# Kernel tuning notes

Measured on AMD Instinct MI355X. Metric: run time of the kernel, lower is better.

Reference implementation:

```python
import jax, jax.numpy as jnp
import numpy as np
import math

B, D_MODEL, H, D_K, L = 24, 128, 8, 16, 512


def setup_inputs() -> dict:
    key = jax.random.key(0)
    ks = jax.random.split(key, 5)
    x = jax.random.normal(ks[0], (B, D_MODEL, L), dtype=jnp.float32)
    Wq = jax.random.normal(ks[1], (H, B, D_K, D_MODEL), dtype=jnp.float32)
    Wk = jax.random.normal(ks[2], (H, B, D_K, D_MODEL), dtype=jnp.float32)
    Wv = jax.random.normal(ks[3], (H, B, D_K, D_MODEL), dtype=jnp.float32)
    Wo = jax.random.normal(ks[4], (B, H * D_K, D_MODEL), dtype=jnp.float32)
    return {"x": x, "Wq": Wq, "Wk": Wk, "Wv": Wv, "Wo": Wo}


def reference(x, Wq, Wk, Wv, Wo):
    # Per-head, per-batch projections: [h,b,k,d] @ [b,d,l] -> [h,b,k,l]
    Q = jnp.einsum('hbkd,bdl->hbkl', Wq, x)
    K = jnp.einsum('hbkd,bdl->hbkl', Wk, x)
    V = jnp.einsum('hbkd,bdl->hbkl', Wv, x)
    # scores[h,b,l,m] = Q[:, :, :, l] . K[:, :, :, m]; torch softmax dim=1 of
    # the [B, L, L] score -> softmax over the QUERY axis l (axis=2 here).
    scores = jnp.einsum('hbkl,hbkm->hblm', Q, K) / math.sqrt(D_K)
    attn = jax.nn.softmax(scores, axis=2)
    # head_i = V @ attn : [h,b,v,l] @ [h,b,l,m] -> [h,b,v,m]
    heads = jnp.einsum('hbvl,hblm->hbvm', V, attn)
    # concat heads along channel dim: [b, h*v, L]
    head = heads.transpose(1, 0, 2, 3).reshape(B, H * D_K, L)
    # out = Wo @ head : [b, h*v, d_model] treated as [b,128,128] @ [b,128,L]
    out = jnp.einsum('bod,bdl->bol', Wo, head)
    return out
```

## Files before the change

### kernel.cpp

```cpp
#include <hip/hip_runtime.h>
#include <math.h>

#define NB 24
#define DM 128
#define NH 8
#define DK 16
#define LL 512
#define HB (NH * NB)

#define XTH_OFF 0
#define XTL_OFF 3145728
#define WHI_OFF 6291456
#define WLO_OFF 8650752
#define WOB_OFF 11010048
#define QB_OFF  11796480
#define KB_OFF  18087936
#define VB_OFF  24379392
#define HT_OFF  27525120

typedef __attribute__((ext_vector_type(8))) short bf16x8;
typedef __attribute__((ext_vector_type(4))) float f32x4;
typedef __attribute__((ext_vector_type(4))) int   i32x4;

#define MFMA  __builtin_amdgcn_mfma_f32_16x16x32_bf16
#define EXP2  __builtin_amdgcn_exp2f
#define BPERM __builtin_amdgcn_ds_bpermute

static __device__ __forceinline__ unsigned bfr(float x) {
    return (__float_as_uint(x) + 0x8000u) & 0xffff0000u;
}
static __device__ __forceinline__ unsigned pk2(unsigned e, unsigned o) {
    return (e >> 16) | o;
}

__global__ __launch_bounds__(256)
void prep(const float* __restrict__ x,
          const float* __restrict__ Wq,
          const float* __restrict__ Wk,
          const float* __restrict__ Wv,
          const float* __restrict__ Wo,
          unsigned short* __restrict__ xthi,
          unsigned short* __restrict__ xtlo,
          unsigned short* __restrict__ whi,
          unsigned short* __restrict__ wlo,
          unsigned short* __restrict__ wob)
{
    __shared__ float T[128][65];
    const int bid = blockIdx.x, tid = threadIdx.x;

    if (bid < 192) {
        const int b = bid >> 3, lc = bid & 7;
        const float* __restrict__ xb = x + (size_t)b * 65536 + lc * 64;
        #pragma unroll
        for (int i = 0; i < 32; ++i) {
            const int idx = i * 256 + tid;
            T[idx >> 6][idx & 63] = xb[(size_t)(idx >> 6) * LL + (idx & 63)];
        }
        __syncthreads();
        #pragma unroll
        for (int i = 0; i < 32; ++i) {
            const int idx = i * 256 + tid;
            const int l = idx >> 7, d = idx & 127;
            const float v = T[d][l];
            const unsigned h = bfr(v);
            const size_t o = (size_t)b * 65536 + (size_t)(lc * 64 + l) * DM + d;
            xthi[o] = (unsigned short)(h >> 16);
            xtlo[o] = (unsigned short)(bfr(v - __uint_as_float(h)) >> 16);
        }
    } else if (bid < 768) {
        const int w = bid - 192, hb = w / 3, mat = w - hb * 3;
        const float* __restrict__ src =
            (mat == 0 ? Wq : (mat == 1 ? Wk : Wv)) + (size_t)hb * 2048;
        unsigned short* __restrict__ dh = whi + (size_t)w * 2048;
        unsigned short* __restrict__ dl = wlo + (size_t)w * 2048;
        for (int i = tid; i < 2048; i += 256) {
            const float v = src[i];
            const unsigned h = bfr(v);
            dh[i] = (unsigned short)(h >> 16);
            dl[i] = (unsigned short)(bfr(v - __uint_as_float(h)) >> 16);
        }
    } else {
        const int w = bid - 768;
        const float* __restrict__ src = Wo + (size_t)w * 4096;
        unsigned short* __restrict__ d = wob + (size_t)w * 4096;
        for (int i = tid; i < 4096; i += 256)
            d[i] = (unsigned short)(bfr(src[i]) >> 16);
    }
}

__global__ __launch_bounds__(256)
void qkv_mfma(const unsigned short* __restrict__ xthi,
              const unsigned short* __restrict__ xtlo,
              const unsigned short* __restrict__ whi,
              const unsigned short* __restrict__ wlo,
              unsigned short* __restrict__ qb,
              unsigned short* __restrict__ kb,
              unsigned short* __restrict__ vb)
{
    const int blk  = blockIdx.x;
    const int nc   = blk & 1;
    const int hm   = blk >> 1;
    const int mat  = hm % 3;
    const int hb   = hm / 3;
    const int b    = hb % NB;
    const int wv   = threadIdx.x >> 6;
    const int lane = threadIdx.x & 63;
    const int g = lane >> 4, mR = lane & 15;
    const int l0 = nc * 256 + wv * 64;

    const unsigned short* __restrict__ wA = whi + (size_t)hm * 2048 + mR * 128 + g * 8;
    const unsigned short* __restrict__ wB = wlo + (size_t)hm * 2048 + mR * 128 + g * 8;
    const unsigned short* __restrict__ xh = xthi + (size_t)b * 65536 + g * 8;
    const unsigned short* __restrict__ xl = xtlo + (size_t)b * 65536 + g * 8;

    f32x4 C[4];
    #pragma unroll
    for (int t = 0; t < 4; ++t) C[t] = (f32x4){0.f, 0.f, 0.f, 0.f};

    #pragma unroll
    for (int kk = 0; kk < 4; ++kk) {
        const bf16x8 aH = *(const bf16x8*)(wA + kk * 32);
        const bf16x8 aL = *(const bf16x8*)(wB + kk * 32);
        #pragma unroll
        for (int t = 0; t < 4; ++t) {
            const size_t lo_ = (size_t)(l0 + t * 16 + mR) * DM + kk * 32;
            const bf16x8 bH = *(const bf16x8*)(xh + lo_);
            const bf16x8 bL = *(const bf16x8*)(xl + lo_);
            C[t] = MFMA(aH, bH, C[t], 0, 0, 0);
            C[t] = MFMA(aH, bL, C[t], 0, 0, 0);
            C[t] = MFMA(aL, bH, C[t], 0, 0, 0);
        }
    }

    if (mat == 2) {
        unsigned short* __restrict__ vo = vb + (size_t)hb * 8192;
        #pragma unroll
        for (int t = 0; t < 4; ++t) {
            const int l = l0 + t * 16 + mR;
            #pragma unroll
            for (int i = 0; i < 4; ++i)
                vo[(size_t)(4 * g + i) * LL + l] =
                    (unsigned short)(bfr(C[t][i]) >> 16);
        }
    } else {
        const float scale = (mat == 1) ? (0.25f * 1.44269504f) : 1.0f;
        unsigned short* __restrict__ dst =
            (mat == 0 ? qb : kb) + (size_t)hb * LL * 32;
        #pragma unroll
        for (int t = 0; t < 4; ++t) {
            const int l = l0 + t * 16 + mR;
            ushort4 hi4, lo4;
            #pragma unroll
            for (int i = 0; i < 4; ++i) {
                const float v = C[t][i] * scale;
                const unsigned h = bfr(v);
                const unsigned lw = bfr(v - __uint_as_float(h));
                ((unsigned short*)&hi4)[i] = (unsigned short)(h >> 16);
                ((unsigned short*)&lo4)[i] = (unsigned short)(lw >> 16);
            }
            *(ushort4*)(dst + (size_t)l * 32 + 4 * g)      = hi4;
            *(ushort4*)(dst + (size_t)l * 32 + 16 + 4 * g) = lo4;
        }
    }
}

static __device__ __forceinline__ void soft_pv(
    const f32x4& s0, const f32x4& s1, float tm, float& bar, float& sm,
    f32x4& O, const bf16x8& aV, int aLo, int aHi, bool up)
{
    const float nb = fmaxf(bar, tm + 32.f);
    const float f  = EXP2(bar - nb);
    bar = nb;
    const unsigned u0 = bfr(EXP2(s0[0]-nb)), u1 = bfr(EXP2(s0[1]-nb));
    const unsigned u2 = bfr(EXP2(s0[2]-nb)), u3 = bfr(EXP2(s0[3]-nb));
    const unsigned w0 = bfr(EXP2(s1[0]-nb)), w1 = bfr(EXP2(s1[1]-nb));
    const unsigned w2 = bfr(EXP2(s1[2]-nb)), w3 = bfr(EXP2(s1[3]-nb));
    const float sacc =
        ((__uint_as_float(u0) + __uint_as_float(u1)) +
         (__uint_as_float(u2) + __uint_as_float(u3))) +
        ((__uint_as_float(w0) + __uint_as_float(w1)) +
         (__uint_as_float(w2) + __uint_as_float(w3)));
    sm = fmaf(sm, f, sacc);
    O *= f;
    const int c0 = (int)pk2(u0, u1), c1 = (int)pk2(u2, u3);
    const int c2 = (int)pk2(w0, w1), c3 = (int)pk2(w2, w3);
    const int p00 = BPERM(aLo, c0), p02 = BPERM(aLo, c2);
    const int p10 = BPERM(aLo, c1), p12 = BPERM(aLo, c3);
    const int p20 = BPERM(aHi, c0), p22 = BPERM(aHi, c2);
    const int p30 = BPERM(aHi, c1), p32 = BPERM(aHi, c3);
    i32x4 bi = { up ? p00 : p02, up ? p10 : p12,
                 up ? p20 : p22, up ? p30 : p32 };
    O = MFMA(aV, __builtin_bit_cast(bf16x8, bi), O, 0, 0, 0);
}

__global__ __launch_bounds__(256)
void attn_mfma(const unsigned short* __restrict__ qb,
               const unsigned short* __restrict__ kb,
               const unsigned short* __restrict__ vb,
               unsigned short* __restrict__ ht)
{
    const int hb   = blockIdx.x >> 2;
    const int mc   = blockIdx.x & 3;
    const int tid  = threadIdx.x;
    const int wave = tid >> 6;
    const int lane = tid & 63;
    const int g    = lane >> 4;
    const int mR   = lane & 15;
    const int mb   = mc * 128 + wave * 32;

    const unsigned short* Kr0 = kb + ((size_t)hb * LL + mb + mR) * 32;
    const unsigned short* Kr1 = Kr0 + 16 * 32;
    const bf16x8 bK0  = *(const bf16x8*)(Kr0 + g * 8);
    const bf16x8 bK0s = *(const bf16x8*)(Kr0 + (g ^ 2) * 8);
    const bf16x8 bK1  = *(const bf16x8*)(Kr1 + g * 8);
    const bf16x8 bK1s = *(const bf16x8*)(Kr1 + (g ^ 2) * 8);

    const unsigned short* qrow = qb + ((size_t)hb * LL + mR) * 32 + g * 8;
    const unsigned short* vrow = vb + ((size_t)hb * DK + mR) * LL + g * 8;

    f32x4 O0 = {0.f,0.f,0.f,0.f}, O1 = {0.f,0.f,0.f,0.f};
    float bar0 = -1e30f, bar1 = -1e30f, sm0 = 0.f, sm1 = 0.f;

    const int aLo = ((g & 1) * 32 + mR) * 4;
    const int aHi = aLo + 64;
    const bool up = (g < 2);

    for (int l = 0; l < LL; l += 32) {
        const bf16x8 aQ0 = *(const bf16x8*)(qrow + (size_t)l * 32);
        const bf16x8 aQ1 = *(const bf16x8*)(qrow + (size_t)(l + 16) * 32);

        const f32x4 z = {0.f,0.f,0.f,0.f};
        f32x4 sA0 = MFMA(aQ0, bK0, z, 0,0,0);  sA0 = MFMA(aQ0, bK0s, sA0, 0,0,0);
        f32x4 sB0 = MFMA(aQ0, bK1, z, 0,0,0);  sB0 = MFMA(aQ0, bK1s, sB0, 0,0,0);
        f32x4 sA1 = MFMA(aQ1, bK0, z, 0,0,0);  sA1 = MFMA(aQ1, bK0s, sA1, 0,0,0);
        f32x4 sB1 = MFMA(aQ1, bK1, z, 0,0,0);  sB1 = MFMA(aQ1, bK1s, sB1, 0,0,0);

        float tmA = fmaxf(fmaxf(fmaxf(sA0[0],sA0[1]), fmaxf(sA0[2],sA0[3])),
                          fmaxf(fmaxf(sA1[0],sA1[1]), fmaxf(sA1[2],sA1[3])));
        float tmB = fmaxf(fmaxf(fmaxf(sB0[0],sB0[1]), fmaxf(sB0[2],sB0[3])),
                          fmaxf(fmaxf(sB1[0],sB1[1]), fmaxf(sB1[2],sB1[3])));
        tmA = fmaxf(tmA, __shfl_xor(tmA, 16, 64));
        tmA = fmaxf(tmA, __shfl_xor(tmA, 32, 64));
        tmB = fmaxf(tmB, __shfl_xor(tmB, 16, 64));
        tmB = fmaxf(tmB, __shfl_xor(tmB, 32, 64));

        if (__any(tmA + 64.f > bar0) || __any(tmB + 64.f > bar1)) {
            const bf16x8 aV = *(const bf16x8*)(vrow + l);
            soft_pv(sA0, sA1, tmA, bar0, sm0, O0, aV, aLo, aHi, up);
            soft_pv(sB0, sB1, tmB, bar1, sm1, O1, aV, aLo, aHi, up);
        }
    }

    sm0 += __shfl_xor(sm0, 16, 64);  sm0 += __shfl_xor(sm0, 32, 64);
    sm1 += __shfl_xor(sm1, 16, 64);  sm1 += __shfl_xor(sm1, 32, 64);
    const float i0 = 1.f / sm0, i1 = 1.f / sm1;

    const int h = hb / NB, bb = hb % NB;
    unsigned short* __restrict__ ho =
        ht + (size_t)bb * 65536 + (size_t)(mb + mR) * DM + h * 16 + 4 * g;
    ushort4 p0, p1;
    #pragma unroll
    for (int i = 0; i < 4; ++i) {
        ((unsigned short*)&p0)[i] = (unsigned short)(bfr(O0[i] * i0) >> 16);
        ((unsigned short*)&p1)[i] = (unsigned short)(bfr(O1[i] * i1) >> 16);
    }
    *(ushort4*)ho              = p0;
    *(ushort4*)(ho + 16 * DM)  = p1;
}

__global__ __launch_bounds__(256)
void out_mfma(const unsigned short* __restrict__ wob,
              const unsigned short* __restrict__ ht,
              float* __restrict__ out)
{
    const int blk  = blockIdx.x;
    const int b    = blk >> 5;
    const int mq   = (blk >> 4) & 1;
    const int nq   = blk & 15;
    const int wv   = threadIdx.x >> 6;
    const int lane = threadIdx.x & 63;
    const int g = lane >> 4, mR = lane & 15;
    const int m0 = (mq * 4 + wv) * 16;
    const int n0 = nq * 32;

    const unsigned short* __restrict__ A =
        wob + (size_t)b * 16384 + (size_t)(m0 + mR) * DM + g * 8;
    const unsigned short* __restrict__ B = ht + (size_t)b * 65536 + g * 8;

    f32x4 C0 = {0.f,0.f,0.f,0.f}, C1 = {0.f,0.f,0.f,0.f};
    #pragma unroll
    for (int kk = 0; kk < 4; ++kk) {
        const bf16x8 aW = *(const bf16x8*)(A + kk * 32);
        const bf16x8 b0 = *(const bf16x8*)(B + (size_t)(n0 + mR) * DM + kk * 32);
        const bf16x8 b1 = *(const bf16x8*)(B + (size_t)(n0 + 16 + mR) * DM + kk * 32);
        C0 = MFMA(aW, b0, C0, 0, 0, 0);
        C1 = MFMA(aW, b1, C1, 0, 0, 0);
    }

    float* __restrict__ ob = out + (size_t)b * 65536 + (size_t)(m0 + 4 * g) * LL;
    #pragma unroll
    for (int i = 0; i < 4; ++i) {
        ob[(size_t)i * LL + n0 + mR]      = C0[i];
        ob[(size_t)i * LL + n0 + 16 + mR] = C1[i];
    }
}

extern "C" void kernel_launch(void* const* d_in, const int* in_sizes, int n_in,
                              void* d_out, int out_size, void* d_ws, size_t ws_size,
                              hipStream_t stream) {
    const float* x  = (const float*)d_in[0];
    const float* Wq = (const float*)d_in[1];
    const float* Wk = (const float*)d_in[2];
    const float* Wv = (const float*)d_in[3];
    const float* Wo = (const float*)d_in[4];
    float* out = (float*)d_out;

    char* ws = (char*)d_ws;
    unsigned short* xthi = (unsigned short*)(ws + XTH_OFF);
    unsigned short* xtlo = (unsigned short*)(ws + XTL_OFF);
    unsigned short* whi  = (unsigned short*)(ws + WHI_OFF);
    unsigned short* wlo  = (unsigned short*)(ws + WLO_OFF);
    unsigned short* wob  = (unsigned short*)(ws + WOB_OFF);
    unsigned short* qb   = (unsigned short*)(ws + QB_OFF);
    unsigned short* kb   = (unsigned short*)(ws + KB_OFF);
    unsigned short* vb   = (unsigned short*)(ws + VB_OFF);
    unsigned short* ht   = (unsigned short*)(ws + HT_OFF);

    prep     <<<864,     256, 0, stream>>>(x, Wq, Wk, Wv, Wo, xthi, xtlo, whi, wlo, wob);
    qkv_mfma <<<HB * 6,  256, 0, stream>>>(xthi, xtlo, whi, wlo, qb, kb, vb);
    attn_mfma<<<HB * 4,  256, 0, stream>>>(qb, kb, vb, ht);
    out_mfma <<<NB * 32, 256, 0, stream>>>(wob, ht, out);
}
```

Measured before the change: 127.3 us.

## Fuse weight bf16 splitting into GEMMs and use two-pass exact softmax max

Stops pre-converting Wq/Wk/Wv/Wo in the prep kernel. The QKV and output GEMM kernels now load the fp32 weights directly and split or convert them to bf16 in registers, which removes the weight workspace traffic and shrinks prep to the x transpose only. The x transpose now uses a smaller LDS tile and packed 32-bit stores. Attention replaces the online-rescaled softmax with its conditional skip by a first pass that computes the exact column max from cheap scores, then a second pass doing exp, a packed v_cvt_pk_bf16_f32 conversion and the PV MFMA without bpermute shuffles. The price is recomputing QK scores twice and redundant weight conversion across blocks.

```diff
diff --git a/kernel.cpp b/kernel.cpp
--- a/kernel.cpp
+++ b/kernel.cpp
@@ -10,13 +10,10 @@
 
 #define XTH_OFF 0
 #define XTL_OFF 3145728
-#define WHI_OFF 6291456
-#define WLO_OFF 8650752
-#define WOB_OFF 11010048
-#define QB_OFF  11796480
-#define KB_OFF  18087936
-#define VB_OFF  24379392
-#define HT_OFF  27525120
+#define QB_OFF  6291456
+#define KB_OFF  12582912
+#define VB_OFF  18874368
+#define HT_OFF  22020096
 
 typedef __attribute__((ext_vector_type(8))) short bf16x8;
 typedef __attribute__((ext_vector_type(4))) float f32x4;
@@ -24,75 +21,78 @@
 
 #define MFMA  __builtin_amdgcn_mfma_f32_16x16x32_bf16
 #define EXP2  __builtin_amdgcn_exp2f
-#define BPERM __builtin_amdgcn_ds_bpermute
 
 static __device__ __forceinline__ unsigned bfr(float x) {
     return (__float_as_uint(x) + 0x8000u) & 0xffff0000u;
 }
-static __device__ __forceinline__ unsigned pk2(unsigned e, unsigned o) {
-    return (e >> 16) | o;
+
+static __device__ __forceinline__ unsigned cvtpk(float a, float b) {
+    unsigned r;
+    asm("v_cvt_pk_bf16_f32 %0, %1, %2" : "=v"(r) : "v"(a), "v"(b));
+    return r;
+}
+
+static __device__ __forceinline__ void wsplit(const float* __restrict__ p,
+                                              bf16x8& aH, bf16x8& aL) {
+    const float4 f0 = *(const float4*)p;
+    const float4 f1 = *(const float4*)(p + 4);
+    const float f[8] = {f0.x, f0.y, f0.z, f0.w, f1.x, f1.y, f1.z, f1.w};
+    i32x4 h, l;
+    #pragma unroll
+    for (int q = 0; q < 4; ++q) {
+        const unsigned h0 = bfr(f[2 * q]), h1 = bfr(f[2 * q + 1]);
+        const unsigned e0 = bfr(f[2 * q]     - __uint_as_float(h0));
+        const unsigned e1 = bfr(f[2 * q + 1] - __uint_as_float(h1));
+        h[q] = (int)((h0 >> 16) | (h1 & 0xffff0000u));
+        l[q] = (int)((e0 >> 16) | (e1 & 0xffff0000u));
+    }
+    aH = __builtin_bit_cast(bf16x8, h);
+    aL = __builtin_bit_cast(bf16x8, l);
 }
 
 __global__ __launch_bounds__(256)
 void prep(const float* __restrict__ x,
-          const float* __restrict__ Wq,
-          const float* __restrict__ Wk,
-          const float* __restrict__ Wv,
-          const float* __restrict__ Wo,
           unsigned short* __restrict__ xthi,
-          unsigned short* __restrict__ xtlo,
-          unsigned short* __restrict__ whi,
-          unsigned short* __restrict__ wlo,
-          unsigned short* __restrict__ wob)
-{
-    __shared__ float T[128][65];
+          unsigned short* __restrict__ xtlo)
+{
+    __shared__ float T[64][65];
     const int bid = blockIdx.x, tid = threadIdx.x;
-
-    if (bid < 192) {
-        const int b = bid >> 3, lc = bid & 7;
-        const float* __restrict__ xb = x + (size_t)b * 65536 + lc * 64;
-        #pragma unroll
-        for (int i = 0; i < 32; ++i) {
+    const int b = bid >> 3, lc = bid & 7;
+
+    #pragma unroll
+    for (int half = 0; half < 2; ++half) {
+        const int d0 = half << 6;
+        const float* __restrict__ xb =
+            x + (size_t)b * 65536 + (size_t)d0 * LL + lc * 64;
+        if (half) __syncthreads();
+        #pragma unroll
+        for (int i = 0; i < 16; ++i) {
             const int idx = i * 256 + tid;
             T[idx >> 6][idx & 63] = xb[(size_t)(idx >> 6) * LL + (idx & 63)];
         }
         __syncthreads();
         #pragma unroll
-        for (int i = 0; i < 32; ++i) {
-            const int idx = i * 256 + tid;
-            const int l = idx >> 7, d = idx & 127;
-            const float v = T[d][l];
-            const unsigned h = bfr(v);
-            const size_t o = (size_t)b * 65536 + (size_t)(lc * 64 + l) * DM + d;
-            xthi[o] = (unsigned short)(h >> 16);
-            xtlo[o] = (unsigned short)(bfr(v - __uint_as_float(h)) >> 16);
-        }
-    } else if (bid < 768) {
-        const int w = bid - 192, hb = w / 3, mat = w - hb * 3;
-        const float* __restrict__ src =
-            (mat == 0 ? Wq : (mat == 1 ? Wk : Wv)) + (size_t)hb * 2048;
-        unsigned short* __restrict__ dh = whi + (size_t)w * 2048;
-        unsigned short* __restrict__ dl = wlo + (size_t)w * 2048;
-        for (int i = tid; i < 2048; i += 256) {
-            const float v = src[i];
-            const unsigned h = bfr(v);
-            dh[i] = (unsigned short)(h >> 16);
-            dl[i] = (unsigned short)(bfr(v - __uint_as_float(h)) >> 16);
-        }
-    } else {
-        const int w = bid - 768;
-        const float* __restrict__ src = Wo + (size_t)w * 4096;
-        unsigned short* __restrict__ d = wob + (size_t)w * 4096;
-        for (int i = tid; i < 4096; i += 256)
-            d[i] = (unsigned short)(bfr(src[i]) >> 16);
+        for (int i = 0; i < 8; ++i) {
+            const int idx = (i * 256 + tid) * 2;
+            const int l = idx >> 6, dd = idx & 63;
+            const float v0 = T[dd][l], v1 = T[dd + 1][l];
+            const unsigned h0 = bfr(v0), h1 = bfr(v1);
+            const unsigned e0 = bfr(v0 - __uint_as_float(h0));
+            const unsigned e1 = bfr(v1 - __uint_as_float(h1));
+            const size_t o = (size_t)b * 65536 +
+                             (size_t)(lc * 64 + l) * DM + d0 + dd;
+            *(unsigned*)(xthi + o) = (h0 >> 16) | (h1 & 0xffff0000u);
+            *(unsigned*)(xtlo + o) = (e0 >> 16) | (e1 & 0xffff0000u);
+        }
     }
 }
 
 __global__ __launch_bounds__(256)
 void qkv_mfma(const unsigned short* __restrict__ xthi,
               const unsigned short* __restrict__ xtlo,
-              const unsigned short* __restrict__ whi,
-              const unsigned short* __restrict__ wlo,
+              const float* __restrict__ Wq,
+              const float* __restrict__ Wk,
+              const float* __restrict__ Wv,
               unsigned short* __restrict__ qb,
               unsigned short* __restrict__ kb,
               unsigned short* __restrict__ vb)
@@ -108,8 +108,9 @@
     const int g = lane >> 4, mR = lane & 15;
     const int l0 = nc * 256 + wv * 64;
 
-    const unsigned short* __restrict__ wA = whi + (size_t)hm * 2048 + mR * 128 + g * 8;
-    const unsigned short* __restrict__ wB = wlo + (size_t)hm * 2048 + mR * 128 + g * 8;
+    const float* __restrict__ wp =
+        (mat == 0 ? Wq : (mat == 1 ? Wk : Wv)) +
+        (size_t)hb * 2048 + mR * 128 + g * 8;
     const unsigned short* __restrict__ xh = xthi + (size_t)b * 65536 + g * 8;
     const unsigned short* __restrict__ xl = xtlo + (size_t)b * 65536 + g * 8;
 
@@ -119,8 +120,8 @@
 
     #pragma unroll
     for (int kk = 0; kk < 4; ++kk) {
-        const bf16x8 aH = *(const bf16x8*)(wA + kk * 32);
-        const bf16x8 aL = *(const bf16x8*)(wB + kk * 32);
+        bf16x8 aH, aL;
+        wsplit(wp + kk * 32, aH, aL);
         #pragma unroll
         for (int t = 0; t < 4; ++t) {
             const size_t lo_ = (size_t)(l0 + t * 16 + mR) * DM + kk * 32;
@@ -164,32 +165,17 @@
     }
 }
 
-static __device__ __forceinline__ void soft_pv(
-    const f32x4& s0, const f32x4& s1, float tm, float& bar, float& sm,
-    f32x4& O, const bf16x8& aV, int aLo, int aHi, bool up)
-{
-    const float nb = fmaxf(bar, tm + 32.f);
-    const float f  = EXP2(bar - nb);
-    bar = nb;
-    const unsigned u0 = bfr(EXP2(s0[0]-nb)), u1 = bfr(EXP2(s0[1]-nb));
-    const unsigned u2 = bfr(EXP2(s0[2]-nb)), u3 = bfr(EXP2(s0[3]-nb));
-    const unsigned w0 = bfr(EXP2(s1[0]-nb)), w1 = bfr(EXP2(s1[1]-nb));
-    const unsigned w2 = bfr(EXP2(s1[2]-nb)), w3 = bfr(EXP2(s1[3]-nb));
-    const float sacc =
-        ((__uint_as_float(u0) + __uint_as_float(u1)) +
-         (__uint_as_float(u2) + __uint_as_float(u3))) +
-        ((__uint_as_float(w0) + __uint_as_float(w1)) +
-         (__uint_as_float(w2) + __uint_as_float(w3)));
-    sm = fmaf(sm, f, sacc);
-    O *= f;
-    const int c0 = (int)pk2(u0, u1), c1 = (int)pk2(u2, u3);
-    const int c2 = (int)pk2(w0, w1), c3 = (int)pk2(w2, w3);
-    const int p00 = BPERM(aLo, c0), p02 = BPERM(aLo, c2);
-    const int p10 = BPERM(aLo, c1), p12 = BPERM(aLo, c3);
-    const int p20 = BPERM(aHi, c0), p22 = BPERM(aHi, c2);
-    const int p30 = BPERM(aHi, c1), p32 = BPERM(aHi, c3);
-    i32x4 bi = { up ? p00 : p02, up ? p10 : p12,
-                 up ? p20 : p22, up ? p30 : p32 };
+static __device__ __forceinline__ void pv_acc(
+    const f32x4& s0, const f32x4& s1, float M, float& sm,
+    f32x4& O, const bf16x8& aV)
+{
+    const float e0 = EXP2(s0[0] - M), e1 = EXP2(s0[1] - M);
+    const float e2 = EXP2(s0[2] - M), e3 = EXP2(s0[3] - M);
+    const float e4 = EXP2(s1[0] - M), e5 = EXP2(s1[1] - M);
+    const float e6 = EXP2(s1[2] - M), e7 = EXP2(s1[3] - M);
+    sm += ((e0 + e1) + (e2 + e3)) + ((e4 + e5) + (e6 + e7));
+    i32x4 bi = { (int)cvtpk(e0, e1), (int)cvtpk(e2, e3),
+                 (int)cvtpk(e4, e5), (int)cvtpk(e6, e7) };
     O = MFMA(aV, __builtin_bit_cast(bf16x8, bi), O, 0, 0, 0);
 }
 
@@ -201,54 +187,60 @@
 {
     const int hb   = blockIdx.x >> 2;
     const int mc   = blockIdx.x & 3;
-    const int tid  = threadIdx.x;
-    const int wave = tid >> 6;
-    const int lane = tid & 63;
+    const int wave = (threadIdx.x >> 6);
+    const int lane = threadIdx.x & 63;
     const int g    = lane >> 4;
     const int mR   = lane & 15;
     const int mb   = mc * 128 + wave * 32;
 
     const unsigned short* Kr0 = kb + ((size_t)hb * LL + mb + mR) * 32;
     const unsigned short* Kr1 = Kr0 + 16 * 32;
-    const bf16x8 bK0  = *(const bf16x8*)(Kr0 + g * 8);
-    const bf16x8 bK0s = *(const bf16x8*)(Kr0 + (g ^ 2) * 8);
-    const bf16x8 bK1  = *(const bf16x8*)(Kr1 + g * 8);
-    const bf16x8 bK1s = *(const bf16x8*)(Kr1 + (g ^ 2) * 8);
-
-    const unsigned short* qrow = qb + ((size_t)hb * LL + mR) * 32 + g * 8;
-    const unsigned short* vrow = vb + ((size_t)hb * DK + mR) * LL + g * 8;
+    const bf16x8 K0  = *(const bf16x8*)(Kr0 + g * 8);
+    const bf16x8 K0s = *(const bf16x8*)(Kr0 + (g ^ 2) * 8);
+    const bf16x8 K1  = *(const bf16x8*)(Kr1 + g * 8);
+    const bf16x8 K1s = *(const bf16x8*)(Kr1 + (g ^ 2) * 8);
+
+    const int rA = 8 * (mR >> 2) + (mR & 3);
+    const unsigned short* qrowA = qb + ((size_t)hb * LL + rA) * 32 + g * 8;
+    const unsigned short* qrowB = qrowA + 4 * 32;
+    const unsigned short* vrow  = vb + ((size_t)hb * DK + mR) * LL + g * 8;
+
+    float M0 = -1e30f, M1 = -1e30f;
+    for (int l = 0; l < LL; l += 32) {
+        const bf16x8 aQ0 = *(const bf16x8*)(qrowA + (size_t)l * 32);
+        const bf16x8 aQ1 = *(const bf16x8*)(qrowB + (size_t)l * 32);
+        const f32x4 z = {0.f,0.f,0.f,0.f};
+        const f32x4 sA0 = MFMA(aQ0, K0, z, 0,0,0);
+        const f32x4 sB0 = MFMA(aQ0, K1, z, 0,0,0);
+        const f32x4 sA1 = MFMA(aQ1, K0, z, 0,0,0);
+        const f32x4 sB1 = MFMA(aQ1, K1, z, 0,0,0);
+        const float tA = fmaxf(fmaxf(fmaxf(sA0[0],sA0[1]), fmaxf(sA0[2],sA0[3])),
+                               fmaxf(fmaxf(sA1[0],sA1[1]), fmaxf(sA1[2],sA1[3])));
+        const float tB = fmaxf(fmaxf(fmaxf(sB0[0],sB0[1]), fmaxf(sB0[2],sB0[3])),
+                               fmaxf(fmaxf(sB1[0],sB1[1]), fmaxf(sB1[2],sB1[3])));
+        M0 = fmaxf(M0, tA);
+        M1 = fmaxf(M1, tB);
+    }
+    M0 = fmaxf(M0, __shfl_xor(M0, 16, 64));
+    M0 = fmaxf(M0, __shfl_xor(M0, 32, 64));
+    M1 = fmaxf(M1, __shfl_xor(M1, 16, 64));
+    M1 = fmaxf(M1, __shfl_xor(M1, 32, 64));
 
     f32x4 O0 = {0.f,0.f,0.f,0.f}, O1 = {0.f,0.f,0.f,0.f};
-    float bar0 = -1e30f, bar1 = -1e30f, sm0 = 0.f, sm1 = 0.f;
-
-    const int aLo = ((g & 1) * 32 + mR) * 4;
-    const int aHi = aLo + 64;
-    const bool up = (g < 2);
-
+    float sm0 = 0.f, sm1 = 0.f;
     for (int l = 0; l < LL; l += 32) {
-        const bf16x8 aQ0 = *(const bf16x8*)(qrow + (size_t)l * 32);
-        const bf16x8 aQ1 = *(const bf16x8*)(qrow + (size_t)(l + 16) * 32);
+        const bf16x8 aQ0 = *(const bf16x8*)(qrowA + (size_t)l * 32);
+        const bf16x8 aQ1 = *(const bf16x8*)(qrowB + (size_t)l * 32);
+        const bf16x8 aV  = *(const bf16x8*)(vrow + l);
 
         const f32x4 z = {0.f,0.f,0.f,0.f};
-        f32x4 sA0 = MFMA(aQ0, bK0, z, 0,0,0);  sA0 = MFMA(aQ0, bK0s, sA0, 0,0,0);
-        f32x4 sB0 = MFMA(aQ0, bK1, z, 0,0,0);  sB0 = MFMA(aQ0, bK1s, sB0, 0,0,0);
-        f32x4 sA1 = MFMA(aQ1, bK0, z, 0,0,0);  sA1 = MFMA(aQ1, bK0s, sA1, 0,0,0);
-        f32x4 sB1 = MFMA(aQ1, bK1, z, 0,0,0);  sB1 = MFMA(aQ1, bK1s, sB1, 0,0,0);
-
-        float tmA = fmaxf(fmaxf(fmaxf(sA0[0],sA0[1]), fmaxf(sA0[2],sA0[3])),
-                          fmaxf(fmaxf(sA1[0],sA1[1]), fmaxf(sA1[2],sA1[3])));
-        float tmB = fmaxf(fmaxf(fmaxf(sB0[0],sB0[1]), fmaxf(sB0[2],sB0[3])),
-                          fmaxf(fmaxf(sB1[0],sB1[1]), fmaxf(sB1[2],sB1[3])));
-        tmA = fmaxf(tmA, __shfl_xor(tmA, 16, 64));
-        tmA = fmaxf(tmA, __shfl_xor(tmA, 32, 64));
-        tmB = fmaxf(tmB, __shfl_xor(tmB, 16, 64));
-        tmB = fmaxf(tmB, __shfl_xor(tmB, 32, 64));
-
-        if (__any(tmA + 64.f > bar0) || __any(tmB + 64.f > bar1)) {
-            const bf16x8 aV = *(const bf16x8*)(vrow + l);
-            soft_pv(sA0, sA1, tmA, bar0, sm0, O0, aV, aLo, aHi, up);
-            soft_pv(sB0, sB1, tmB, bar1, sm1, O1, aV, aLo, aHi, up);
-        }
+        f32x4 sA0 = MFMA(aQ0, K0, z, 0,0,0);   sA0 = MFMA(aQ0, K0s, sA0, 0,0,0);
+        f32x4 sB0 = MFMA(aQ0, K1, z, 0,0,0);   sB0 = MFMA(aQ0, K1s, sB0, 0,0,0);
+        f32x4 sA1 = MFMA(aQ1, K0, z, 0,0,0);   sA1 = MFMA(aQ1, K0s, sA1, 0,0,0);
+        f32x4 sB1 = MFMA(aQ1, K1, z, 0,0,0);   sB1 = MFMA(aQ1, K1s, sB1, 0,0,0);
+
+        pv_acc(sA0, sA1, M0, sm0, O0, aV);
+        pv_acc(sB0, sB1, M1, sm1, O1, aV);
     }
 
     sm0 += __shfl_xor(sm0, 16, 64);  sm0 += __shfl_xor(sm0, 32, 64);
@@ -269,7 +261,7 @@
 }
 
 __global__ __launch_bounds__(256)
-void out_mfma(const unsigned short* __restrict__ wob,
+void out_mfma(const float* __restrict__ Wo,
               const unsigned short* __restrict__ ht,
               float* __restrict__ out)
 {
@@ -283,14 +275,21 @@
     const int m0 = (mq * 4 + wv) * 16;
     const int n0 = nq * 32;
 
-    const unsigned short* __restrict__ A =
-        wob + (size_t)b * 16384 + (size_t)(m0 + mR) * DM + g * 8;
+    const float* __restrict__ A =
+        Wo + (size_t)b * 16384 + (size_t)(m0 + mR) * DM + g * 8;
     const unsigned short* __restrict__ B = ht + (size_t)b * 65536 + g * 8;
 
     f32x4 C0 = {0.f,0.f,0.f,0.f}, C1 = {0.f,0.f,0.f,0.f};
     #pragma unroll
     for (int kk = 0; kk < 4; ++kk) {
-        const bf16x8 aW = *(const bf16x8*)(A + kk * 32);
+        const float4 f0 = *(const float4*)(A + kk * 32);
+        const float4 f1 = *(const float4*)(A + kk * 32 + 4);
+        i32x4 w;
+        w[0] = (int)cvtpk(f0.x, f0.y);
+        w[1] = (int)cvtpk(f0.z, f0.w);
+        w[2] = (int)cvtpk(f1.x, f1.y);
+        w[3] = (int)cvtpk(f1.z, f1.w);
+        const bf16x8 aW = __builtin_bit_cast(bf16x8, w);
         const bf16x8 b0 = *(const bf16x8*)(B + (size_t)(n0 + mR) * DM + kk * 32);
         const bf16x8 b1 = *(const bf16x8*)(B + (size_t)(n0 + 16 + mR) * DM + kk * 32);
         C0 = MFMA(aW, b0, C0, 0, 0, 0);
@@ -318,16 +317,13 @@
     char* ws = (char*)d_ws;
     unsigned short* xthi = (unsigned short*)(ws + XTH_OFF);
     unsigned short* xtlo = (unsigned short*)(ws + XTL_OFF);
-    unsigned short* whi  = (unsigned short*)(ws + WHI_OFF);
-    unsigned short* wlo  = (unsigned short*)(ws + WLO_OFF);
-    unsigned short* wob  = (unsigned short*)(ws + WOB_OFF);
     unsigned short* qb   = (unsigned short*)(ws + QB_OFF);
     unsigned short* kb   = (unsigned short*)(ws + KB_OFF);
     unsigned short* vb   = (unsigned short*)(ws + VB_OFF);
     unsigned short* ht   = (unsigned short*)(ws + HT_OFF);
 
-    prep     <<<864,     256, 0, stream>>>(x, Wq, Wk, Wv, Wo, xthi, xtlo, whi, wlo, wob);
-    qkv_mfma <<<HB * 6,  256, 0, stream>>>(xthi, xtlo, whi, wlo, qb, kb, vb);
+    prep     <<<192,     256, 0, stream>>>(x, xthi, xtlo);
+    qkv_mfma <<<HB * 6,  256, 0, stream>>>(xthi, xtlo, Wq, Wk, Wv, qb, kb, vb);
     attn_mfma<<<HB * 4,  256, 0, stream>>>(qb, kb, vb, ht);
-    out_mfma <<<NB * 32, 256, 0, stream>>>(wob, ht, out);
-}
+    out_mfma <<<NB * 32, 256, 0, stream>>>(Wo, ht, out);
+}
```

Result: faster. 124.4 us (-2.3%).
